# Performance work log

Measured on AMD Instinct MI355X. Metric: run time of the kernel, lower is better.

## Reference

```python
import jax, jax.numpy as jnp
import numpy as np

V, BLOCK, L, H, E, B, T = 1024, 2048, 4, 8, 512, 4, 2048
D = E // H  # head dim = 64

def setup_inputs() -> dict:
    key = jax.random.key(0)
    ks = jax.random.split(key, 8)
    s = 0.02
    return {
        "idx": jax.random.randint(ks[0], (B, T), 0, V),
        "wte": jax.random.normal(ks[1], (V, E), jnp.float32) * s,
        "wpe": jax.random.normal(ks[2], (BLOCK, E), jnp.float32) * s,
        "ln1_w": jnp.ones((L, E), jnp.float32),
        "ln1_b": jnp.zeros((L, E), jnp.float32),
        "attn_w": jax.random.normal(ks[3], (L, 3 * E, E), jnp.float32) * s,
        "attn_b": jnp.zeros((L, 3 * E), jnp.float32),
        "proj_w": jax.random.normal(ks[4], (L, E, E), jnp.float32) * s,
        "proj_b": jnp.zeros((L, E), jnp.float32),
        "ln2_w": jnp.ones((L, E), jnp.float32),
        "ln2_b": jnp.zeros((L, E), jnp.float32),
        "fc_w": jax.random.normal(ks[5], (L, 4 * E, E), jnp.float32) * s,
        "fc_b": jnp.zeros((L, 4 * E), jnp.float32),
        "fc2_w": jax.random.normal(ks[6], (L, E, 4 * E), jnp.float32) * s,
        "fc2_b": jnp.zeros((L, E), jnp.float32),
        "lnf_w": jnp.ones((E,), jnp.float32),
        "lnf_b": jnp.zeros((E,), jnp.float32),
    }

def layer_norm(x, w, b, eps=1e-5):
    mu = jnp.mean(x, axis=-1, keepdims=True)
    var = jnp.var(x, axis=-1, keepdims=True)
    return (x - mu) * jax.lax.rsqrt(var + eps) * w + b

def reference(idx, wte, wpe, ln1_w, ln1_b, attn_w, attn_b, proj_w, proj_b,
              ln2_w, ln2_b, fc_w, fc_b, fc2_w, fc2_b, lnf_w, lnf_b):
    b, t = idx.shape
    x = wte[idx] + wpe[:t]  # (B,T,E)
    causal = jnp.tril(jnp.ones((t, t), bool))
    scale = 1.0 / np.sqrt(D)

    def block(x, p):
        l1w, l1b, aw, ab, pw, pb, l2w, l2b, fw, fb, f2w, f2b = p
        h = layer_norm(x, l1w, l1b)
        qkv = h @ aw.T + ab  # (B,T,3E)
        q, k, v = jnp.split(qkv, 3, axis=-1)
        q = q.reshape(b, t, H, D)
        k = k.reshape(b, t, H, D)
        v = v.reshape(b, t, H, D)
        att = jnp.einsum('bqhd,bkhd->bhqk', q, k) * scale
        att = jnp.where(causal, att, -jnp.inf)
        att = jax.nn.softmax(att, axis=-1)
        y = jnp.einsum('bhqk,bkhd->bqhd', att, v).reshape(b, t, E)
        x = x + y @ pw.T + pb
        h2 = layer_norm(x, l2w, l2b)
        h2 = jax.nn.gelu(h2 @ fw.T + fb, approximate=False)
        x = x + h2 @ f2w.T + f2b
        return x, None

    params = (ln1_w, ln1_b, attn_w, attn_b, proj_w, proj_b,
              ln2_w, ln2_b, fc_w, fc_b, fc2_w, fc2_b)
    x, _ = jax.lax.scan(block, x, params)
    x = layer_norm(x, lnf_w, lnf_b)
    logits = x @ wte.T  # tied lm_head
    return logits
```

## Files before the change

kernel.cpp:

```cpp
#include <hip/hip_runtime.h>
#include <hip/hip_bf16.h>
#include <math.h>

#define B_ 4
#define T_ 2048
#define E_ 512
#define H_ 8
#define D_ 64
#define L_ 4
#define V_ 1024
#define NROWS (B_*T_)
#define KBLK 64
#define KVPAD 72
#define PPAD 72

typedef __hip_bfloat16 bf16;
typedef __attribute__((ext_vector_type(8))) short bf16x8;
typedef __attribute__((ext_vector_type(4))) float f32x4;

__device__ __forceinline__ short f2bf_s(float f) {
    union { bf16 h; short s; } t; t.h = __float2bfloat16(f); return t.s;
}

__device__ __forceinline__ void gload_lds16(const bf16* g, bf16* l) {
    __builtin_amdgcn_global_load_lds((const __attribute__((address_space(1))) void*)g,
                                     (__attribute__((address_space(3))) void*)l, 16, 0, 0);
}

__device__ __forceinline__ float gelu_fast(float v) {
    float u = v * (0.7978845608028654f * (1.0f + 0.044715f * v * v));
    float t = 1.0f - 2.0f / (__expf(2.0f * u) + 1.0f);
    return 0.5f * v * (1.0f + t);
}

__global__ void f2bf_all(const float* __restrict__ s0, const float* __restrict__ s1,
                         const float* __restrict__ s2, const float* __restrict__ s3,
                         const float* __restrict__ s4, bf16* __restrict__ dst) {
    size_t gi = (size_t)blockIdx.x * 1024 + threadIdx.x * 4;
    const float* src; size_t off;
    if (blockIdx.x < 3072)       { src = s0; off = gi; }
    else if (blockIdx.x < 4096)  { src = s1; off = gi - (size_t)3072 * 1024; }
    else if (blockIdx.x < 8192)  { src = s2; off = gi - (size_t)4096 * 1024; }
    else if (blockIdx.x < 12288) { src = s3; off = gi - (size_t)8192 * 1024; }
    else                         { src = s4; off = gi - (size_t)12288 * 1024; }
    float4 v = *(const float4*)(src + off);
    union { bf16 h[4]; uint2 u; } t;
    t.h[0] = __float2bfloat16(v.x); t.h[1] = __float2bfloat16(v.y);
    t.h[2] = __float2bfloat16(v.z); t.h[3] = __float2bfloat16(v.w);
    *(uint2*)(dst + gi) = t.u;
}

__global__ void embed_kernel(const int* __restrict__ idx, const float* __restrict__ wte,
                             const float* __restrict__ wpe, float* __restrict__ x) {
    int i = (blockIdx.x * blockDim.x + threadIdx.x) * 4;
    int row = i >> 9;
    int e = i & (E_ - 1);
    int t = row & (T_ - 1);
    int id = idx[row];
    float4 a = *(const float4*)(wte + (size_t)id * E_ + e);
    float4 p = *(const float4*)(wpe + (size_t)t * E_ + e);
    a.x += p.x; a.y += p.y; a.z += p.z; a.w += p.w;
    *(float4*)(x + i) = a;
}

__global__ __launch_bounds__(512) void layernorm_kernel(const float* __restrict__ x,
                                 const float* __restrict__ w, const float* __restrict__ b,
                                 bf16* __restrict__ out) {
    int wid = threadIdx.x >> 6, lane = threadIdx.x & 63;
    int row = blockIdx.x * 8 + wid;
    const float* xr = x + (size_t)row * E_ + lane * 8;
    float4 a0 = *(const float4*)xr;
    float4 a1 = *(const float4*)(xr + 4);
    float s = (a0.x + a0.y) + (a0.z + a0.w) + (a1.x + a1.y) + (a1.z + a1.w);
    float q = a0.x*a0.x + a0.y*a0.y + a0.z*a0.z + a0.w*a0.w
            + a1.x*a1.x + a1.y*a1.y + a1.z*a1.z + a1.w*a1.w;
    #pragma unroll
    for (int st = 1; st < 64; st <<= 1) { s += __shfl_xor(s, st); q += __shfl_xor(q, st); }
    float mean = s * (1.0f / E_);
    float var = q * (1.0f / E_) - mean * mean;
    float rstd = rsqrtf(var + 1e-5f);
    float4 w0 = *(const float4*)(w + lane * 8), w1 = *(const float4*)(w + lane * 8 + 4);
    float4 b0 = *(const float4*)(b + lane * 8), b1 = *(const float4*)(b + lane * 8 + 4);
    union { bf16 h[8]; uint4 u; } o;
    o.h[0] = __float2bfloat16((a0.x - mean) * rstd * w0.x + b0.x);
    o.h[1] = __float2bfloat16((a0.y - mean) * rstd * w0.y + b0.y);
    o.h[2] = __float2bfloat16((a0.z - mean) * rstd * w0.z + b0.z);
    o.h[3] = __float2bfloat16((a0.w - mean) * rstd * w0.w + b0.w);
    o.h[4] = __float2bfloat16((a1.x - mean) * rstd * w1.x + b1.x);
    o.h[5] = __float2bfloat16((a1.y - mean) * rstd * w1.y + b1.y);
    o.h[6] = __float2bfloat16((a1.z - mean) * rstd * w1.z + b1.z);
    o.h[7] = __float2bfloat16((a1.w - mean) * rstd * w1.w + b1.w);
    *(uint4*)(out + (size_t)row * E_ + lane * 8) = o.u;
}

template<int ACT, int OMODE, bool BIAS, bool QKV>
__global__ __launch_bounds__(256) void gemm_mfma(const bf16* __restrict__ A, const bf16* __restrict__ W,
        const float* __restrict__ bias, float* __restrict__ Cf, bf16* __restrict__ Cb,
        bf16* __restrict__ Vt, int M, int N, int K) {
    __shared__ __align__(16) bf16 As[2][128][32];
    __shared__ __align__(16) bf16 Bs[2][128][32];
    int tid = threadIdx.x;
    int lane = tid & 63, wid = tid >> 6;
    int wm = (wid >> 1) * 64, wn = (wid & 1) * 64;
    int m0 = blockIdx.y * 128, n0 = blockIdx.x * 128;

    int srow = wid * 32 + (lane >> 2);
    int scol = (lane & 3) * 8;
    const bf16* ga = A + (size_t)(m0 + srow) * K + scol;
    const bf16* gb = W + (size_t)(n0 + srow) * K + scol;
    int fr = lane & 15, fk = (lane >> 4) * 8;

    f32x4 acc[4][4];
    #pragma unroll
    for (int i = 0; i < 4; ++i)
        #pragma unroll
        for (int j = 0; j < 4; ++j) acc[i][j] = (f32x4){0.f, 0.f, 0.f, 0.f};

    gload_lds16(ga,          &As[0][wid * 32][0]);
    gload_lds16(ga + 16 * K, &As[0][wid * 32 + 16][0]);
    gload_lds16(gb,          &Bs[0][wid * 32][0]);
    gload_lds16(gb + 16 * K, &Bs[0][wid * 32 + 16][0]);
    __syncthreads();

    const int nst = K >> 5;
    for (int t = 0; t < nst; ++t) {
        const int cur = t & 1;
        if (t + 1 < nst) {
            const bf16* ga2 = ga + (t + 1) * 32;
            const bf16* gb2 = gb + (t + 1) * 32;
            gload_lds16(ga2,          &As[cur ^ 1][wid * 32][0]);
            gload_lds16(ga2 + 16 * K, &As[cur ^ 1][wid * 32 + 16][0]);
            gload_lds16(gb2,          &Bs[cur ^ 1][wid * 32][0]);
            gload_lds16(gb2 + 16 * K, &Bs[cur ^ 1][wid * 32 + 16][0]);
        }
        bf16x8 af[4], bff[4];
        #pragma unroll
        for (int i = 0; i < 4; ++i) af[i]  = *(const bf16x8*)&As[cur][wm + i * 16 + fr][fk];
        #pragma unroll
        for (int j = 0; j < 4; ++j) bff[j] = *(const bf16x8*)&Bs[cur][wn + j * 16 + fr][fk];
        #pragma unroll
        for (int i = 0; i < 4; ++i)
            #pragma unroll
            for (int j = 0; j < 4; ++j)
                acc[i][j] = __builtin_amdgcn_mfma_f32_16x16x32_bf16(af[i], bff[j], acc[i][j], 0, 0, 0);
        __syncthreads();
    }

    int orow = m0 + wm + (lane >> 4) * 4;
    int ocol = n0 + wn + (lane & 15);

    if (QKV && n0 >= 2 * E_) {
        #pragma unroll
        for (int i = 0; i < 4; ++i) {
            int rowb = orow + i * 16;
            int bb = rowb >> 11;
            int t0 = rowb & (T_ - 1);
            #pragma unroll
            for (int j = 0; j < 4; ++j) {
                int col = ocol + j * 16;
                int dg = col - 2 * E_;
                int hh = dg >> 6, dd = dg & 63;
                float bv = BIAS ? bias[col] : 0.0f;
                union { bf16 h[4]; short4 s4; } pk;
                #pragma unroll
                for (int r = 0; r < 4; ++r)
                    pk.h[r] = __float2bfloat16(acc[i][j][r] + bv);
                *(short4*)&Vt[(((size_t)bb * H_ + hh) * D_ + dd) * T_ + t0] = pk.s4;
            }
        }
        return;
    }

    #pragma unroll
    for (int i = 0; i < 4; ++i) {
        #pragma unroll
        for (int j = 0; j < 4; ++j) {
            #pragma unroll
            for (int r = 0; r < 4; ++r) {
                int row = orow + i * 16 + r;
                int col = ocol + j * 16;
                float v = acc[i][j][r];
                if (BIAS) v += bias[col];
                if (ACT == 1) v = gelu_fast(v);
                if (QKV) {
                    if (col < E_) v *= 0.125f;
                    Cb[(size_t)row * (2 * E_) + col] = __float2bfloat16(v);
                } else {
                    size_t off = (size_t)row * N + col;
                    if (OMODE == 0) Cf[off] = v;
                    else if (OMODE == 1) Cb[off] = __float2bfloat16(v);
                    else Cf[off] += v;
                }
            }
        }
    }
}

template<int OMODE, bool BIAS>
__global__ __launch_bounds__(256) void gemm_mfma64(const bf16* __restrict__ A, const bf16* __restrict__ W,
        const float* __restrict__ bias, float* __restrict__ Cf, bf16* __restrict__ Cb,
        int M, int N, int K) {
    __shared__ __align__(16) bf16 As[2][64][32];
    __shared__ __align__(16) bf16 Bs[2][64][32];
    int tid = threadIdx.x;
    int lane = tid & 63, wid = tid >> 6;
    int wm = (wid >> 1) * 32, wn = (wid & 1) * 32;
    int m0 = blockIdx.y * 64, n0 = blockIdx.x * 64;

    int srow = wid * 16 + (lane >> 2);
    int scol = (lane & 3) * 8;
    const bf16* ga = A + (size_t)(m0 + srow) * K + scol;
    const bf16* gb = W + (size_t)(n0 + srow) * K + scol;
    int fr = lane & 15, fk = (lane >> 4) * 8;

    f32x4 acc[2][2];
    #pragma unroll
    for (int i = 0; i < 2; ++i)
        #pragma unroll
        for (int j = 0; j < 2; ++j) acc[i][j] = (f32x4){0.f, 0.f, 0.f, 0.f};

    gload_lds16(ga, &As[0][wid * 16][0]);
    gload_lds16(gb, &Bs[0][wid * 16][0]);
    __syncthreads();

    const int nst = K >> 5;
    for (int t = 0; t < nst; ++t) {
        const int cur = t & 1;
        if (t + 1 < nst) {
            gload_lds16(ga + (t + 1) * 32, &As[cur ^ 1][wid * 16][0]);
            gload_lds16(gb + (t + 1) * 32, &Bs[cur ^ 1][wid * 16][0]);
        }
        bf16x8 af[2], bff[2];
        #pragma unroll
        for (int i = 0; i < 2; ++i) af[i]  = *(const bf16x8*)&As[cur][wm + i * 16 + fr][fk];
        #pragma unroll
        for (int j = 0; j < 2; ++j) bff[j] = *(const bf16x8*)&Bs[cur][wn + j * 16 + fr][fk];
        #pragma unroll
        for (int i = 0; i < 2; ++i)
            #pragma unroll
            for (int j = 0; j < 2; ++j)
                acc[i][j] = __builtin_amdgcn_mfma_f32_16x16x32_bf16(af[i], bff[j], acc[i][j], 0, 0, 0);
        __syncthreads();
    }

    int orow = m0 + wm + (lane >> 4) * 4;
    int ocol = n0 + wn + (lane & 15);
    #pragma unroll
    for (int i = 0; i < 2; ++i) {
        #pragma unroll
        for (int j = 0; j < 2; ++j) {
            #pragma unroll
            for (int r = 0; r < 4; ++r) {
                int row = orow + i * 16 + r;
                int col = ocol + j * 16;
                float v = acc[i][j][r];
                if (BIAS) v += bias[col];
                size_t off = (size_t)row * N + col;
                if (OMODE == 0) Cf[off] = v;
                else if (OMODE == 1) Cb[off] = __float2bfloat16(v);
                else Cf[off] += v;
            }
        }
    }
}

template<bool DOMASK>
__device__ __forceinline__ void attn_tile(
        const short (&Ks)[KBLK][KVPAD], const short (&VsT)[D_][KVPAD],
        short (*Psw)[PPAD], const bf16x8 (&qf)[2],
        float& m_run, float& l_run, f32x4 (&accO)[4],
        int fr, int fg, int k0, int qrow) {
    f32x4 st[4];
    __builtin_amdgcn_s_setprio(1);
    #pragma unroll
    for (int j = 0; j < 4; ++j) {
        f32x4 a = (f32x4){0.f, 0.f, 0.f, 0.f};
        #pragma unroll
        for (int kk = 0; kk < 2; ++kk) {
            bf16x8 kf = *(const bf16x8*)&Ks[j * 16 + fr][kk * 32 + fg * 8];
            a = __builtin_amdgcn_mfma_f32_16x16x32_bf16(kf, qf[kk], a, 0, 0, 0);
        }
        st[j] = a;
    }
    __builtin_amdgcn_s_setprio(0);
    float mx = -INFINITY;
    #pragma unroll
    for (int j = 0; j < 4; ++j)
        #pragma unroll
        for (int r = 0; r < 4; ++r) {
            if (DOMASK && (k0 + j * 16 + fg * 4 + r > qrow)) st[j][r] = -INFINITY;
            mx = fmaxf(mx, st[j][r]);
        }
    mx = fmaxf(mx, __shfl_xor(mx, 16));
    mx = fmaxf(mx, __shfl_xor(mx, 32));
    if (!__all(mx <= m_run + 8.0f)) {
        float mnew = fmaxf(m_run, mx);
        float corr = __expf(m_run - mnew);
        l_run *= corr;
        #pragma unroll
        for (int r = 0; r < 4; ++r) {
            float cr = __shfl(corr, fg * 4 + r);
            #pragma unroll
            for (int n = 0; n < 4; ++n) accO[n][r] *= cr;
        }
        m_run = mnew;
    }
    float rl = 0.0f;
    #pragma unroll
    for (int j = 0; j < 4; ++j) {
        float p0 = __expf(st[j][0] - m_run), p1 = __expf(st[j][1] - m_run);
        float p2 = __expf(st[j][2] - m_run), p3 = __expf(st[j][3] - m_run);
        rl += (p0 + p1) + (p2 + p3);
        short4 pk;
        pk.x = f2bf_s(p0); pk.y = f2bf_s(p1); pk.z = f2bf_s(p2); pk.w = f2bf_s(p3);
        *(short4*)&Psw[fr][j * 16 + fg * 4] = pk;
    }
    rl += __shfl_xor(rl, 16);
    rl += __shfl_xor(rl, 32);
    l_run += rl;
    __builtin_amdgcn_s_setprio(1);
    bf16x8 pa[2];
    #pragma unroll
    for (int kk = 0; kk < 2; ++kk)
        pa[kk] = *(const bf16x8*)&Psw[fr][kk * 32 + fg * 8];
    #pragma unroll
    for (int n = 0; n < 4; ++n)
        #pragma unroll
        for (int kk = 0; kk < 2; ++kk) {
            bf16x8 vb = *(const bf16x8*)&VsT[n * 16 + fr][kk * 32 + fg * 8];
            accO[n] = __builtin_amdgcn_mfma_f32_16x16x32_bf16(pa[kk], vb, accO[n], 0, 0, 0);
        }
    __builtin_amdgcn_s_setprio(0);
}

__global__ __launch_bounds__(256, 4) void attn_mfma(const bf16* __restrict__ qk,
                                                    const bf16* __restrict__ vt,
                                                    bf16* __restrict__ y) {
    __shared__ __align__(16) short Ks[KBLK][KVPAD];
    __shared__ __align__(16) short VsT[D_][KVPAD];
    __shared__ __align__(16) short Ps[4][16][PPAD];
    const int qi = (gridDim.x - 1) - blockIdx.x;
    const int h = blockIdx.y, b = blockIdx.z;
    const int q0 = qi * 64;
    const int tid = threadIdx.x;
    const int lane = tid & 63, wid = tid >> 6;
    const int fr = lane & 15, fg = lane >> 4;
    const int qmin = q0 + wid * 16;
    const int qrow = qmin + fr;

    const int sr0 = tid >> 3;
    const int sc = (tid & 7) * 8;
    const bf16* kst = qk + (size_t)(b * T_ + sr0) * (2 * E_) + E_ + h * D_ + sc;
    const bf16* vst = vt + ((size_t)(b * H_ + h) * D_ + sr0) * T_ + sc;

    const bf16* qbase = qk + (size_t)(b * T_ + qrow) * (2 * E_) + h * D_;
    bf16x8 qf[2];
    #pragma unroll
    for (int kk = 0; kk < 2; ++kk)
        qf[kk] = *(const bf16x8*)(qbase + kk * 32 + fg * 8);

    float m_run = -INFINITY, l_run = 0.0f;
    f32x4 accO[4];
    #pragma unroll
    for (int n = 0; n < 4; ++n) accO[n] = (f32x4){0.f, 0.f, 0.f, 0.f};

    const int ntiles = qi + 1;

    {
        uint4 k0r = *(const uint4*)kst;
        uint4 k1r = *(const uint4*)(kst + 32 * (2 * E_));
        uint4 v0r = *(const uint4*)vst;
        uint4 v1r = *(const uint4*)(vst + 32 * T_);
        *(uint4*)&Ks[sr0][sc] = k0r;  *(uint4*)&Ks[sr0 + 32][sc] = k1r;
        *(uint4*)&VsT[sr0][sc] = v0r; *(uint4*)&VsT[sr0 + 32][sc] = v1r;
    }
    __syncthreads();

    for (int kt = 0; kt < ntiles; ++kt) {
        const bool have_next = (kt + 1 < ntiles);
        uint4 nk0, nk1, nv0, nv1;
        if (have_next) {
            const bf16* kn = kst + (size_t)(kt + 1) * KBLK * (2 * E_);
            const bf16* vn = vst + (kt + 1) * KBLK;
            nk0 = *(const uint4*)kn; nk1 = *(const uint4*)(kn + 32 * (2 * E_));
            nv0 = *(const uint4*)vn; nv1 = *(const uint4*)(vn + 32 * T_);
        }

        if (kt + 1 == ntiles)
            attn_tile<true >(Ks, VsT, Ps[wid], qf, m_run, l_run, accO, fr, fg, kt * KBLK, qrow);
        else
            attn_tile<false>(Ks, VsT, Ps[wid], qf, m_run, l_run, accO, fr, fg, kt * KBLK, qrow);

        __syncthreads();
        if (have_next) {
            *(uint4*)&Ks[sr0][sc] = nk0;  *(uint4*)&Ks[sr0 + 32][sc] = nk1;
            *(uint4*)&VsT[sr0][sc] = nv0; *(uint4*)&VsT[sr0 + 32][sc] = nv1;
            __syncthreads();
        }
    }

    float linv = 1.0f / l_run;
    #pragma unroll
    for (int r = 0; r < 4; ++r) {
        float lr = __shfl(linv, fg * 4 + r);
        int gq = qmin + fg * 4 + r;
        #pragma unroll
        for (int n = 0; n < 4; ++n)
            y[(size_t)(b * T_ + gq) * E_ + h * D_ + n * 16 + fr] =
                __float2bfloat16(accO[n][r] * lr);
    }
}

extern "C" void kernel_launch(void* const* d_in, const int* in_sizes, int n_in,
                              void* d_out, int out_size, void* d_ws, size_t ws_size,
                              hipStream_t stream) {
    const int*   idx    = (const int*)d_in[0];
    const float* wte    = (const float*)d_in[1];
    const float* wpe    = (const float*)d_in[2];
    const float* ln1_w  = (const float*)d_in[3];
    const float* ln1_b  = (const float*)d_in[4];
    const float* attn_w = (const float*)d_in[5];
    const float* attn_b = (const float*)d_in[6];
    const float* proj_w = (const float*)d_in[7];
    const float* proj_b = (const float*)d_in[8];
    const float* ln2_w  = (const float*)d_in[9];
    const float* ln2_b  = (const float*)d_in[10];
    const float* fc_w   = (const float*)d_in[11];
    const float* fc_b   = (const float*)d_in[12];
    const float* fc2_w  = (const float*)d_in[13];
    const float* fc2_b  = (const float*)d_in[14];
    const float* lnf_w  = (const float*)d_in[15];
    const float* lnf_b  = (const float*)d_in[16];
    float* out = (float*)d_out;

    float* x   = (float*)d_ws;
    bf16* hbf  = (bf16*)(x + (size_t)NROWS * E_);
    bf16* big  = hbf + (size_t)NROWS * E_;
    bf16* qkb  = big;
    bf16* vtb  = big + (size_t)NROWS * 2 * E_;
    bf16* wb   = big + (size_t)NROWS * 4 * E_;
    bf16* attn_wb = wb;
    bf16* proj_wb = attn_wb + (size_t)L_ * 3 * E_ * E_;
    bf16* fc_wb   = proj_wb + (size_t)L_ * E_ * E_;
    bf16* fc2_wb  = fc_wb   + (size_t)L_ * 4 * E_ * E_;
    bf16* wte_b   = fc2_wb  + (size_t)L_ * E_ * 4 * E_;

    f2bf_all<<<12800, 256, 0, stream>>>(attn_w, proj_w, fc_w, fc2_w, wte, wb);
    embed_kernel<<<NROWS * E_ / 1024, 256, 0, stream>>>(idx, wte, wpe, x);

    for (int l = 0; l < L_; ++l) {
        layernorm_kernel<<<NROWS / 8, 512, 0, stream>>>(x, ln1_w + l * E_, ln1_b + l * E_, hbf);
        gemm_mfma<0, 1, true, true><<<dim3(3 * E_ / 128, NROWS / 128), 256, 0, stream>>>(
            hbf, attn_wb + (size_t)l * 3 * E_ * E_, attn_b + l * 3 * E_, nullptr, qkb, vtb,
            NROWS, 3 * E_, E_);
        attn_mfma<<<dim3(T_ / 64, H_, B_), 256, 0, stream>>>(qkb, vtb, hbf);
        gemm_mfma64<2, true><<<dim3(E_ / 64, NROWS / 64), 256, 0, stream>>>(
            hbf, proj_wb + (size_t)l * E_ * E_, proj_b + l * E_, x, nullptr,
            NROWS, E_, E_);
        layernorm_kernel<<<NROWS / 8, 512, 0, stream>>>(x, ln2_w + l * E_, ln2_b + l * E_, hbf);
        gemm_mfma<1, 1, true, false><<<dim3(4 * E_ / 128, NROWS / 128), 256, 0, stream>>>(
            hbf, fc_wb + (size_t)l * 4 * E_ * E_, fc_b + l * 4 * E_, nullptr, big, nullptr,
            NROWS, 4 * E_, E_);
        gemm_mfma64<2, true><<<dim3(E_ / 64, NROWS / 64), 256, 0, stream>>>(
            big, fc2_wb + (size_t)l * E_ * 4 * E_, fc2_b + l * E_, x, nullptr,
            NROWS, E_, 4 * E_);
    }
    layernorm_kernel<<<NROWS / 8, 512, 0, stream>>>(x, lnf_w, lnf_b, hbf);
    gemm_mfma64<0, false><<<dim3(V_ / 64, NROWS / 64), 256, 0, stream>>>(
        hbf, wte_b, nullptr, out, nullptr, NROWS, V_, E_);
}
```

Baseline: 869.0 us.

## Double attention key block to 128 and move QKV GEMM to 64x64 tiles

The attention kernel now processes 128 keys per tile instead of 64, with wider V and P shared-memory buffers, four-chunk cooperative loads, and half as many tile iterations per query block. Occupancy is lowered from 4 to 3 blocks per SM. The QKV projection moves from the 128x128 GEMM to the 64x64 GEMM, which takes over the V-transpose epilogue, giving more blocks at lower per-block reuse. The goal is fewer barriers and loop overheads in attention and better load balance for QKV, at the cost of more registers and LDS per attention block and extra masked work on the diagonal tile.

```diff
diff --git a/kernel.cpp b/kernel.cpp
--- a/kernel.cpp
+++ b/kernel.cpp
@@ -10,9 +10,10 @@
 #define L_ 4
 #define V_ 1024
 #define NROWS (B_*T_)
-#define KBLK 64
+#define KBLK 128
 #define KVPAD 72
-#define PPAD 72
+#define VPAD 136
+#define PPAD 136
 
 typedef __hip_bfloat16 bf16;
 typedef __attribute__((ext_vector_type(8))) short bf16x8;
@@ -93,10 +94,10 @@
     *(uint4*)(out + (size_t)row * E_ + lane * 8) = o.u;
 }
 
-template<int ACT, int OMODE, bool BIAS, bool QKV>
+template<int ACT, int OMODE, bool BIAS>
 __global__ __launch_bounds__(256) void gemm_mfma(const bf16* __restrict__ A, const bf16* __restrict__ W,
         const float* __restrict__ bias, float* __restrict__ Cf, bf16* __restrict__ Cb,
-        bf16* __restrict__ Vt, int M, int N, int K) {
+        int M, int N, int K) {
     __shared__ __align__(16) bf16 As[2][128][32];
     __shared__ __align__(16) bf16 Bs[2][128][32];
     int tid = threadIdx.x;
@@ -148,15 +149,84 @@
 
     int orow = m0 + wm + (lane >> 4) * 4;
     int ocol = n0 + wn + (lane & 15);
+    #pragma unroll
+    for (int i = 0; i < 4; ++i) {
+        #pragma unroll
+        for (int j = 0; j < 4; ++j) {
+            #pragma unroll
+            for (int r = 0; r < 4; ++r) {
+                int row = orow + i * 16 + r;
+                int col = ocol + j * 16;
+                float v = acc[i][j][r];
+                if (BIAS) v += bias[col];
+                if (ACT == 1) v = gelu_fast(v);
+                size_t off = (size_t)row * N + col;
+                if (OMODE == 0) Cf[off] = v;
+                else if (OMODE == 1) Cb[off] = __float2bfloat16(v);
+                else Cf[off] += v;
+            }
+        }
+    }
+}
+
+template<int OMODE, bool BIAS, bool QKV>
+__global__ __launch_bounds__(256) void gemm_mfma64(const bf16* __restrict__ A, const bf16* __restrict__ W,
+        const float* __restrict__ bias, float* __restrict__ Cf, bf16* __restrict__ Cb,
+        bf16* __restrict__ Vt, int M, int N, int K) {
+    __shared__ __align__(16) bf16 As[2][64][32];
+    __shared__ __align__(16) bf16 Bs[2][64][32];
+    int tid = threadIdx.x;
+    int lane = tid & 63, wid = tid >> 6;
+    int wm = (wid >> 1) * 32, wn = (wid & 1) * 32;
+    int m0 = blockIdx.y * 64, n0 = blockIdx.x * 64;
+
+    int srow = wid * 16 + (lane >> 2);
+    int scol = (lane & 3) * 8;
+    const bf16* ga = A + (size_t)(m0 + srow) * K + scol;
+    const bf16* gb = W + (size_t)(n0 + srow) * K + scol;
+    int fr = lane & 15, fk = (lane >> 4) * 8;
+
+    f32x4 acc[2][2];
+    #pragma unroll
+    for (int i = 0; i < 2; ++i)
+        #pragma unroll
+        for (int j = 0; j < 2; ++j) acc[i][j] = (f32x4){0.f, 0.f, 0.f, 0.f};
+
+    gload_lds16(ga, &As[0][wid * 16][0]);
+    gload_lds16(gb, &Bs[0][wid * 16][0]);
+    __syncthreads();
+
+    const int nst = K >> 5;
+    for (int t = 0; t < nst; ++t) {
+        const int cur = t & 1;
+        if (t + 1 < nst) {
+            gload_lds16(ga + (t + 1) * 32, &As[cur ^ 1][wid * 16][0]);
+            gload_lds16(gb + (t + 1) * 32, &Bs[cur ^ 1][wid * 16][0]);
+        }
+        bf16x8 af[2], bff[2];
+        #pragma unroll
+        for (int i = 0; i < 2; ++i) af[i]  = *(const bf16x8*)&As[cur][wm + i * 16 + fr][fk];
+        #pragma unroll
+        for (int j = 0; j < 2; ++j) bff[j] = *(const bf16x8*)&Bs[cur][wn + j * 16 + fr][fk];
+        #pragma unroll
+        for (int i = 0; i < 2; ++i)
+            #pragma unroll
+            for (int j = 0; j < 2; ++j)
+                acc[i][j] = __builtin_amdgcn_mfma_f32_16x16x32_bf16(af[i], bff[j], acc[i][j], 0, 0, 0);
+        __syncthreads();
+    }
+
+    int orow = m0 + wm + (lane >> 4) * 4;
+    int ocol = n0 + wn + (lane & 15);
 
     if (QKV && n0 >= 2 * E_) {
         #pragma unroll
-        for (int i = 0; i < 4; ++i) {
+        for (int i = 0; i < 2; ++i) {
             int rowb = orow + i * 16;
             int bb = rowb >> 11;
             int t0 = rowb & (T_ - 1);
             #pragma unroll
-            for (int j = 0; j < 4; ++j) {
+            for (int j = 0; j < 2; ++j) {
                 int col = ocol + j * 16;
                 int dg = col - 2 * E_;
                 int hh = dg >> 6, dd = dg & 63;
@@ -172,16 +242,15 @@
     }
 
     #pragma unroll
-    for (int i = 0; i < 4; ++i) {
-        #pragma unroll
-        for (int j = 0; j < 4; ++j) {
+    for (int i = 0; i < 2; ++i) {
+        #pragma unroll
+        for (int j = 0; j < 2; ++j) {
             #pragma unroll
             for (int r = 0; r < 4; ++r) {
                 int row = orow + i * 16 + r;
                 int col = ocol + j * 16;
                 float v = acc[i][j][r];
                 if (BIAS) v += bias[col];
-                if (ACT == 1) v = gelu_fast(v);
                 if (QKV) {
                     if (col < E_) v *= 0.125f;
                     Cb[(size_t)row * (2 * E_) + col] = __float2bfloat16(v);
@@ -196,84 +265,16 @@
     }
 }
 
-template<int OMODE, bool BIAS>
-__global__ __launch_bounds__(256) void gemm_mfma64(const bf16* __restrict__ A, const bf16* __restrict__ W,
-        const float* __restrict__ bias, float* __restrict__ Cf, bf16* __restrict__ Cb,
-        int M, int N, int K) {
-    __shared__ __align__(16) bf16 As[2][64][32];
-    __shared__ __align__(16) bf16 Bs[2][64][32];
-    int tid = threadIdx.x;
-    int lane = tid & 63, wid = tid >> 6;
-    int wm = (wid >> 1) * 32, wn = (wid & 1) * 32;
-    int m0 = blockIdx.y * 64, n0 = blockIdx.x * 64;
-
-    int srow = wid * 16 + (lane >> 2);
-    int scol = (lane & 3) * 8;
-    const bf16* ga = A + (size_t)(m0 + srow) * K + scol;
-    const bf16* gb = W + (size_t)(n0 + srow) * K + scol;
-    int fr = lane & 15, fk = (lane >> 4) * 8;
-
-    f32x4 acc[2][2];
-    #pragma unroll
-    for (int i = 0; i < 2; ++i)
-        #pragma unroll
-        for (int j = 0; j < 2; ++j) acc[i][j] = (f32x4){0.f, 0.f, 0.f, 0.f};
-
-    gload_lds16(ga, &As[0][wid * 16][0]);
-    gload_lds16(gb, &Bs[0][wid * 16][0]);
-    __syncthreads();
-
-    const int nst = K >> 5;
-    for (int t = 0; t < nst; ++t) {
-        const int cur = t & 1;
-        if (t + 1 < nst) {
-            gload_lds16(ga + (t + 1) * 32, &As[cur ^ 1][wid * 16][0]);
-            gload_lds16(gb + (t + 1) * 32, &Bs[cur ^ 1][wid * 16][0]);
-        }
-        bf16x8 af[2], bff[2];
-        #pragma unroll
-        for (int i = 0; i < 2; ++i) af[i]  = *(const bf16x8*)&As[cur][wm + i * 16 + fr][fk];
-        #pragma unroll
-        for (int j = 0; j < 2; ++j) bff[j] = *(const bf16x8*)&Bs[cur][wn + j * 16 + fr][fk];
-        #pragma unroll
-        for (int i = 0; i < 2; ++i)
-            #pragma unroll
-            for (int j = 0; j < 2; ++j)
-                acc[i][j] = __builtin_amdgcn_mfma_f32_16x16x32_bf16(af[i], bff[j], acc[i][j], 0, 0, 0);
-        __syncthreads();
-    }
-
-    int orow = m0 + wm + (lane >> 4) * 4;
-    int ocol = n0 + wn + (lane & 15);
-    #pragma unroll
-    for (int i = 0; i < 2; ++i) {
-        #pragma unroll
-        for (int j = 0; j < 2; ++j) {
-            #pragma unroll
-            for (int r = 0; r < 4; ++r) {
-                int row = orow + i * 16 + r;
-                int col = ocol + j * 16;
-                float v = acc[i][j][r];
-                if (BIAS) v += bias[col];
-                size_t off = (size_t)row * N + col;
-                if (OMODE == 0) Cf[off] = v;
-                else if (OMODE == 1) Cb[off] = __float2bfloat16(v);
-                else Cf[off] += v;
-            }
-        }
-    }
-}
-
 template<bool DOMASK>
 __device__ __forceinline__ void attn_tile(
-        const short (&Ks)[KBLK][KVPAD], const short (&VsT)[D_][KVPAD],
+        const short (&Ks)[KBLK][KVPAD], const short (&VsT)[D_][VPAD],
         short (*Psw)[PPAD], const bf16x8 (&qf)[2],
         float& m_run, float& l_run, f32x4 (&accO)[4],
         int fr, int fg, int k0, int qrow) {
-    f32x4 st[4];
+    f32x4 st[8];
     __builtin_amdgcn_s_setprio(1);
     #pragma unroll
-    for (int j = 0; j < 4; ++j) {
+    for (int j = 0; j < 8; ++j) {
         f32x4 a = (f32x4){0.f, 0.f, 0.f, 0.f};
         #pragma unroll
         for (int kk = 0; kk < 2; ++kk) {
@@ -285,7 +286,7 @@
     __builtin_amdgcn_s_setprio(0);
     float mx = -INFINITY;
     #pragma unroll
-    for (int j = 0; j < 4; ++j)
+    for (int j = 0; j < 8; ++j)
         #pragma unroll
         for (int r = 0; r < 4; ++r) {
             if (DOMASK && (k0 + j * 16 + fg * 4 + r > qrow)) st[j][r] = -INFINITY;
@@ -307,7 +308,7 @@
     }
     float rl = 0.0f;
     #pragma unroll
-    for (int j = 0; j < 4; ++j) {
+    for (int j = 0; j < 8; ++j) {
         float p0 = __expf(st[j][0] - m_run), p1 = __expf(st[j][1] - m_run);
         float p2 = __expf(st[j][2] - m_run), p3 = __expf(st[j][3] - m_run);
         rl += (p0 + p1) + (p2 + p3);
@@ -319,25 +320,25 @@
     rl += __shfl_xor(rl, 32);
     l_run += rl;
     __builtin_amdgcn_s_setprio(1);
-    bf16x8 pa[2];
-    #pragma unroll
-    for (int kk = 0; kk < 2; ++kk)
+    bf16x8 pa[4];
+    #pragma unroll
+    for (int kk = 0; kk < 4; ++kk)
         pa[kk] = *(const bf16x8*)&Psw[fr][kk * 32 + fg * 8];
     #pragma unroll
     for (int n = 0; n < 4; ++n)
         #pragma unroll
-        for (int kk = 0; kk < 2; ++kk) {
+        for (int kk = 0; kk < 4; ++kk) {
             bf16x8 vb = *(const bf16x8*)&VsT[n * 16 + fr][kk * 32 + fg * 8];
             accO[n] = __builtin_amdgcn_mfma_f32_16x16x32_bf16(pa[kk], vb, accO[n], 0, 0, 0);
         }
     __builtin_amdgcn_s_setprio(0);
 }
 
-__global__ __launch_bounds__(256, 4) void attn_mfma(const bf16* __restrict__ qk,
+__global__ __launch_bounds__(256, 3) void attn_mfma(const bf16* __restrict__ qk,
                                                     const bf16* __restrict__ vt,
                                                     bf16* __restrict__ y) {
     __shared__ __align__(16) short Ks[KBLK][KVPAD];
-    __shared__ __align__(16) short VsT[D_][KVPAD];
+    __shared__ __align__(16) short VsT[D_][VPAD];
     __shared__ __align__(16) short Ps[4][16][PPAD];
     const int qi = (gridDim.x - 1) - blockIdx.x;
     const int h = blockIdx.y, b = blockIdx.z;
@@ -348,10 +349,12 @@
     const int qmin = q0 + wid * 16;
     const int qrow = qmin + fr;
 
-    const int sr0 = tid >> 3;
-    const int sc = (tid & 7) * 8;
-    const bf16* kst = qk + (size_t)(b * T_ + sr0) * (2 * E_) + E_ + h * D_ + sc;
-    const bf16* vst = vt + ((size_t)(b * H_ + h) * D_ + sr0) * T_ + sc;
+    const int kr0 = tid >> 3;
+    const int kc = (tid & 7) * 8;
+    const int dv0 = tid >> 4;
+    const int vc = (tid & 15) * 8;
+    const bf16* kst = qk + (size_t)(b * T_ + kr0) * (2 * E_) + E_ + h * D_ + kc;
+    const bf16* vst = vt + ((size_t)(b * H_ + h) * D_ + dv0) * T_ + vc;
 
     const bf16* qbase = qk + (size_t)(b * T_ + qrow) * (2 * E_) + h * D_;
     bf16x8 qf[2];
@@ -364,26 +367,30 @@
     #pragma unroll
     for (int n = 0; n < 4; ++n) accO[n] = (f32x4){0.f, 0.f, 0.f, 0.f};
 
-    const int ntiles = qi + 1;
+    const int ntiles = (qi + 2) >> 1;
 
     {
-        uint4 k0r = *(const uint4*)kst;
-        uint4 k1r = *(const uint4*)(kst + 32 * (2 * E_));
-        uint4 v0r = *(const uint4*)vst;
-        uint4 v1r = *(const uint4*)(vst + 32 * T_);
-        *(uint4*)&Ks[sr0][sc] = k0r;  *(uint4*)&Ks[sr0 + 32][sc] = k1r;
-        *(uint4*)&VsT[sr0][sc] = v0r; *(uint4*)&VsT[sr0 + 32][sc] = v1r;
+        #pragma unroll
+        for (int c = 0; c < 4; ++c) {
+            uint4 kr = *(const uint4*)(kst + (size_t)(c * 32) * (2 * E_));
+            uint4 vr = *(const uint4*)(vst + (size_t)(c * 16) * T_);
+            *(uint4*)&Ks[kr0 + c * 32][kc] = kr;
+            *(uint4*)&VsT[dv0 + c * 16][vc] = vr;
+        }
     }
     __syncthreads();
 
     for (int kt = 0; kt < ntiles; ++kt) {
         const bool have_next = (kt + 1 < ntiles);
-        uint4 nk0, nk1, nv0, nv1;
+        uint4 nk[4], nv[4];
         if (have_next) {
             const bf16* kn = kst + (size_t)(kt + 1) * KBLK * (2 * E_);
             const bf16* vn = vst + (kt + 1) * KBLK;
-            nk0 = *(const uint4*)kn; nk1 = *(const uint4*)(kn + 32 * (2 * E_));
-            nv0 = *(const uint4*)vn; nv1 = *(const uint4*)(vn + 32 * T_);
+            #pragma unroll
+            for (int c = 0; c < 4; ++c) {
+                nk[c] = *(const uint4*)(kn + (size_t)(c * 32) * (2 * E_));
+                nv[c] = *(const uint4*)(vn + (size_t)(c * 16) * T_);
+            }
         }
 
         if (kt + 1 == ntiles)
@@ -393,8 +400,11 @@
 
         __syncthreads();
         if (have_next) {
-            *(uint4*)&Ks[sr0][sc] = nk0;  *(uint4*)&Ks[sr0 + 32][sc] = nk1;
-            *(uint4*)&VsT[sr0][sc] = nv0; *(uint4*)&VsT[sr0 + 32][sc] = nv1;
+            #pragma unroll
+            for (int c = 0; c < 4; ++c) {
+                *(uint4*)&Ks[kr0 + c * 32][kc] = nk[c];
+                *(uint4*)&VsT[dv0 + c * 16][vc] = nv[c];
+            }
             __syncthreads();
         }
     }
@@ -450,22 +460,22 @@
 
     for (int l = 0; l < L_; ++l) {
         layernorm_kernel<<<NROWS / 8, 512, 0, stream>>>(x, ln1_w + l * E_, ln1_b + l * E_, hbf);
-        gemm_mfma<0, 1, true, true><<<dim3(3 * E_ / 128, NROWS / 128), 256, 0, stream>>>(
+        gemm_mfma64<1, true, true><<<dim3(3 * E_ / 64, NROWS / 64), 256, 0, stream>>>(
             hbf, attn_wb + (size_t)l * 3 * E_ * E_, attn_b + l * 3 * E_, nullptr, qkb, vtb,
             NROWS, 3 * E_, E_);
         attn_mfma<<<dim3(T_ / 64, H_, B_), 256, 0, stream>>>(qkb, vtb, hbf);
-        gemm_mfma64<2, true><<<dim3(E_ / 64, NROWS / 64), 256, 0, stream>>>(
-            hbf, proj_wb + (size_t)l * E_ * E_, proj_b + l * E_, x, nullptr,
+        gemm_mfma64<2, true, false><<<dim3(E_ / 64, NROWS / 64), 256, 0, stream>>>(
+            hbf, proj_wb + (size_t)l * E_ * E_, proj_b + l * E_, x, nullptr, nullptr,
             NROWS, E_, E_);
         layernorm_kernel<<<NROWS / 8, 512, 0, stream>>>(x, ln2_w + l * E_, ln2_b + l * E_, hbf);
-        gemm_mfma<1, 1, true, false><<<dim3(4 * E_ / 128, NROWS / 128), 256, 0, stream>>>(
-            hbf, fc_wb + (size_t)l * 4 * E_ * E_, fc_b + l * 4 * E_, nullptr, big, nullptr,
+        gemm_mfma<1, 1, true><<<dim3(4 * E_ / 128, NROWS / 128), 256, 0, stream>>>(
+            hbf, fc_wb + (size_t)l * 4 * E_ * E_, fc_b + l * 4 * E_, nullptr, big,
             NROWS, 4 * E_, E_);
-        gemm_mfma64<2, true><<<dim3(E_ / 64, NROWS / 64), 256, 0, stream>>>(
-            big, fc2_wb + (size_t)l * E_ * 4 * E_, fc2_b + l * E_, x, nullptr,
+        gemm_mfma64<2, true, false><<<dim3(E_ / 64, NROWS / 64), 256, 0, stream>>>(
+            big, fc2_wb + (size_t)l * E_ * 4 * E_, fc2_b + l * E_, x, nullptr, nullptr,
             NROWS, E_, 4 * E_);
     }
     layernorm_kernel<<<NROWS / 8, 512, 0, stream>>>(x, lnf_w, lnf_b, hbf);
-    gemm_mfma64<0, false><<<dim3(V_ / 64, NROWS / 64), 256, 0, stream>>>(
-        hbf, wte_b, nullptr, out, nullptr, NROWS, V_, E_);
-}
+    gemm_mfma64<0, false, false><<<dim3(V_ / 64, NROWS / 64), 256, 0, stream>>>(
+        hbf, wte_b, nullptr, out, nullptr, nullptr, NROWS, V_, E_);
+}
```

After: 1.202 ms. 1.38x slower.

## Double-buffer attention K/V tiles and move QKV GEMM to 64x64 tiles

Applied to the files above, without the earlier changes.

The attention kernel now keeps two LDS buffers for K and V^T, so the next tile's registers are written into the spare buffer right after compute. This removes one of the two block barriers per iteration, at the cost of more shared memory and a lower occupancy hint (3 instead of 4 blocks). The QKV projection GEMM moves from the 128x128-tile kernel to the 64x64-tile kernel, with the QKV-specific epilogue (V transpose and Q scaling) carried over. That gives four times as many blocks and better CU fill, but less data reuse per block.

```diff
diff --git a/kernel.cpp b/kernel.cpp
--- a/kernel.cpp
+++ b/kernel.cpp
@@ -93,10 +93,10 @@
     *(uint4*)(out + (size_t)row * E_ + lane * 8) = o.u;
 }
 
-template<int ACT, int OMODE, bool BIAS, bool QKV>
+template<int ACT, int OMODE, bool BIAS>
 __global__ __launch_bounds__(256) void gemm_mfma(const bf16* __restrict__ A, const bf16* __restrict__ W,
         const float* __restrict__ bias, float* __restrict__ Cf, bf16* __restrict__ Cb,
-        bf16* __restrict__ Vt, int M, int N, int K) {
+        int M, int N, int K) {
     __shared__ __align__(16) bf16 As[2][128][32];
     __shared__ __align__(16) bf16 Bs[2][128][32];
     int tid = threadIdx.x;
@@ -148,15 +148,84 @@
 
     int orow = m0 + wm + (lane >> 4) * 4;
     int ocol = n0 + wn + (lane & 15);
+    #pragma unroll
+    for (int i = 0; i < 4; ++i) {
+        #pragma unroll
+        for (int j = 0; j < 4; ++j) {
+            #pragma unroll
+            for (int r = 0; r < 4; ++r) {
+                int row = orow + i * 16 + r;
+                int col = ocol + j * 16;
+                float v = acc[i][j][r];
+                if (BIAS) v += bias[col];
+                if (ACT == 1) v = gelu_fast(v);
+                size_t off = (size_t)row * N + col;
+                if (OMODE == 0) Cf[off] = v;
+                else if (OMODE == 1) Cb[off] = __float2bfloat16(v);
+                else Cf[off] += v;
+            }
+        }
+    }
+}
+
+template<int OMODE, bool BIAS, bool QKV>
+__global__ __launch_bounds__(256) void gemm_mfma64(const bf16* __restrict__ A, const bf16* __restrict__ W,
+        const float* __restrict__ bias, float* __restrict__ Cf, bf16* __restrict__ Cb,
+        bf16* __restrict__ Vt, int M, int N, int K) {
+    __shared__ __align__(16) bf16 As[2][64][32];
+    __shared__ __align__(16) bf16 Bs[2][64][32];
+    int tid = threadIdx.x;
+    int lane = tid & 63, wid = tid >> 6;
+    int wm = (wid >> 1) * 32, wn = (wid & 1) * 32;
+    int m0 = blockIdx.y * 64, n0 = blockIdx.x * 64;
+
+    int srow = wid * 16 + (lane >> 2);
+    int scol = (lane & 3) * 8;
+    const bf16* ga = A + (size_t)(m0 + srow) * K + scol;
+    const bf16* gb = W + (size_t)(n0 + srow) * K + scol;
+    int fr = lane & 15, fk = (lane >> 4) * 8;
+
+    f32x4 acc[2][2];
+    #pragma unroll
+    for (int i = 0; i < 2; ++i)
+        #pragma unroll
+        for (int j = 0; j < 2; ++j) acc[i][j] = (f32x4){0.f, 0.f, 0.f, 0.f};
+
+    gload_lds16(ga, &As[0][wid * 16][0]);
+    gload_lds16(gb, &Bs[0][wid * 16][0]);
+    __syncthreads();
+
+    const int nst = K >> 5;
+    for (int t = 0; t < nst; ++t) {
+        const int cur = t & 1;
+        if (t + 1 < nst) {
+            gload_lds16(ga + (t + 1) * 32, &As[cur ^ 1][wid * 16][0]);
+            gload_lds16(gb + (t + 1) * 32, &Bs[cur ^ 1][wid * 16][0]);
+        }
+        bf16x8 af[2], bff[2];
+        #pragma unroll
+        for (int i = 0; i < 2; ++i) af[i]  = *(const bf16x8*)&As[cur][wm + i * 16 + fr][fk];
+        #pragma unroll
+        for (int j = 0; j < 2; ++j) bff[j] = *(const bf16x8*)&Bs[cur][wn + j * 16 + fr][fk];
+        #pragma unroll
+        for (int i = 0; i < 2; ++i)
+            #pragma unroll
+            for (int j = 0; j < 2; ++j)
+                acc[i][j] = __builtin_amdgcn_mfma_f32_16x16x32_bf16(af[i], bff[j], acc[i][j], 0, 0, 0);
+        __syncthreads();
+    }
+
+    int orow = m0 + wm + (lane >> 4) * 4;
+    int ocol = n0 + wn + (lane & 15);
 
     if (QKV && n0 >= 2 * E_) {
         #pragma unroll
-        for (int i = 0; i < 4; ++i) {
+        for (int i = 0; i < 2; ++i) {
             int rowb = orow + i * 16;
             int bb = rowb >> 11;
             int t0 = rowb & (T_ - 1);
             #pragma unroll
-            for (int j = 0; j < 4; ++j) {
+            for (int j = 0; j < 2; ++j) {
                 int col = ocol + j * 16;
                 int dg = col - 2 * E_;
                 int hh = dg >> 6, dd = dg & 63;
@@ -172,16 +241,15 @@
     }
 
     #pragma unroll
-    for (int i = 0; i < 4; ++i) {
-        #pragma unroll
-        for (int j = 0; j < 4; ++j) {
+    for (int i = 0; i < 2; ++i) {
+        #pragma unroll
+        for (int j = 0; j < 2; ++j) {
             #pragma unroll
             for (int r = 0; r < 4; ++r) {
                 int row = orow + i * 16 + r;
                 int col = ocol + j * 16;
                 float v = acc[i][j][r];
                 if (BIAS) v += bias[col];
-                if (ACT == 1) v = gelu_fast(v);
                 if (QKV) {
                     if (col < E_) v *= 0.125f;
                     Cb[(size_t)row * (2 * E_) + col] = __float2bfloat16(v);
@@ -196,74 +264,6 @@
     }
 }
 
-template<int OMODE, bool BIAS>
-__global__ __launch_bounds__(256) void gemm_mfma64(const bf16* __restrict__ A, const bf16* __restrict__ W,
-        const float* __restrict__ bias, float* __restrict__ Cf, bf16* __restrict__ Cb,
-        int M, int N, int K) {
-    __shared__ __align__(16) bf16 As[2][64][32];
-    __shared__ __align__(16) bf16 Bs[2][64][32];
-    int tid = threadIdx.x;
-    int lane = tid & 63, wid = tid >> 6;
-    int wm = (wid >> 1) * 32, wn = (wid & 1) * 32;
-    int m0 = blockIdx.y * 64, n0 = blockIdx.x * 64;
-
-    int srow = wid * 16 + (lane >> 2);
-    int scol = (lane & 3) * 8;
-    const bf16* ga = A + (size_t)(m0 + srow) * K + scol;
-    const bf16* gb = W + (size_t)(n0 + srow) * K + scol;
-    int fr = lane & 15, fk = (lane >> 4) * 8;
-
-    f32x4 acc[2][2];
-    #pragma unroll
-    for (int i = 0; i < 2; ++i)
-        #pragma unroll
-        for (int j = 0; j < 2; ++j) acc[i][j] = (f32x4){0.f, 0.f, 0.f, 0.f};
-
-    gload_lds16(ga, &As[0][wid * 16][0]);
-    gload_lds16(gb, &Bs[0][wid * 16][0]);
-    __syncthreads();
-
-    const int nst = K >> 5;
-    for (int t = 0; t < nst; ++t) {
-        const int cur = t & 1;
-        if (t + 1 < nst) {
-            gload_lds16(ga + (t + 1) * 32, &As[cur ^ 1][wid * 16][0]);
-            gload_lds16(gb + (t + 1) * 32, &Bs[cur ^ 1][wid * 16][0]);
-        }
-        bf16x8 af[2], bff[2];
-        #pragma unroll
-        for (int i = 0; i < 2; ++i) af[i]  = *(const bf16x8*)&As[cur][wm + i * 16 + fr][fk];
-        #pragma unroll
-        for (int j = 0; j < 2; ++j) bff[j] = *(const bf16x8*)&Bs[cur][wn + j * 16 + fr][fk];
-        #pragma unroll
-        for (int i = 0; i < 2; ++i)
-            #pragma unroll
-            for (int j = 0; j < 2; ++j)
-                acc[i][j] = __builtin_amdgcn_mfma_f32_16x16x32_bf16(af[i], bff[j], acc[i][j], 0, 0, 0);
-        __syncthreads();
-    }
-
-    int orow = m0 + wm + (lane >> 4) * 4;
-    int ocol = n0 + wn + (lane & 15);
-    #pragma unroll
-    for (int i = 0; i < 2; ++i) {
-        #pragma unroll
-        for (int j = 0; j < 2; ++j) {
-            #pragma unroll
-            for (int r = 0; r < 4; ++r) {
-                int row = orow + i * 16 + r;
-                int col = ocol + j * 16;
-                float v = acc[i][j][r];
-                if (BIAS) v += bias[col];
-                size_t off = (size_t)row * N + col;
-                if (OMODE == 0) Cf[off] = v;
-                else if (OMODE == 1) Cb[off] = __float2bfloat16(v);
-                else Cf[off] += v;
-            }
-        }
-    }
-}
-
 template<bool DOMASK>
 __device__ __forceinline__ void attn_tile(
         const short (&Ks)[KBLK][KVPAD], const short (&VsT)[D_][KVPAD],
@@ -333,11 +333,11 @@
     __builtin_amdgcn_s_setprio(0);
 }
 
-__global__ __launch_bounds__(256, 4) void attn_mfma(const bf16* __restrict__ qk,
+__global__ __launch_bounds__(256, 3) void attn_mfma(const bf16* __restrict__ qk,
                                                     const bf16* __restrict__ vt,
                                                     bf16* __restrict__ y) {
-    __shared__ __align__(16) short Ks[KBLK][KVPAD];
-    __shared__ __align__(16) short VsT[D_][KVPAD];
+    __shared__ __align__(16) short Ks[2][KBLK][KVPAD];
+    __shared__ __align__(16) short VsT[2][D_][KVPAD];
     __shared__ __align__(16) short Ps[4][16][PPAD];
     const int qi = (gridDim.x - 1) - blockIdx.x;
     const int h = blockIdx.y, b = blockIdx.z;
@@ -371,12 +371,13 @@
         uint4 k1r = *(const uint4*)(kst + 32 * (2 * E_));
         uint4 v0r = *(const uint4*)vst;
         uint4 v1r = *(const uint4*)(vst + 32 * T_);
-        *(uint4*)&Ks[sr0][sc] = k0r;  *(uint4*)&Ks[sr0 + 32][sc] = k1r;
-        *(uint4*)&VsT[sr0][sc] = v0r; *(uint4*)&VsT[sr0 + 32][sc] = v1r;
+        *(uint4*)&Ks[0][sr0][sc] = k0r;  *(uint4*)&Ks[0][sr0 + 32][sc] = k1r;
+        *(uint4*)&VsT[0][sr0][sc] = v0r; *(uint4*)&VsT[0][sr0 + 32][sc] = v1r;
     }
     __syncthreads();
 
     for (int kt = 0; kt < ntiles; ++kt) {
+        const int cur = kt & 1;
         const bool have_next = (kt + 1 < ntiles);
         uint4 nk0, nk1, nv0, nv1;
         if (have_next) {
@@ -387,16 +388,16 @@
         }
 
         if (kt + 1 == ntiles)
-            attn_tile<true >(Ks, VsT, Ps[wid], qf, m_run, l_run, accO, fr, fg, kt * KBLK, qrow);
+            attn_tile<true >(Ks[cur], VsT[cur], Ps[wid], qf, m_run, l_run, accO, fr, fg, kt * KBLK, qrow);
         else
-            attn_tile<false>(Ks, VsT, Ps[wid], qf, m_run, l_run, accO, fr, fg, kt * KBLK, qrow);
-
+            attn_tile<false>(Ks[cur], VsT[cur], Ps[wid], qf, m_run, l_run, accO, fr, fg, kt * KBLK, qrow);
+
+        if (have_next) {
+            const int nxt = cur ^ 1;
+            *(uint4*)&Ks[nxt][sr0][sc] = nk0;  *(uint4*)&Ks[nxt][sr0 + 32][sc] = nk1;
+            *(uint4*)&VsT[nxt][sr0][sc] = nv0; *(uint4*)&VsT[nxt][sr0 + 32][sc] = nv1;
+        }
         __syncthreads();
-        if (have_next) {
-            *(uint4*)&Ks[sr0][sc] = nk0;  *(uint4*)&Ks[sr0 + 32][sc] = nk1;
-            *(uint4*)&VsT[sr0][sc] = nv0; *(uint4*)&VsT[sr0 + 32][sc] = nv1;
-            __syncthreads();
-        }
     }
 
     float linv = 1.0f / l_run;
@@ -450,22 +451,22 @@
 
     for (int l = 0; l < L_; ++l) {
         layernorm_kernel<<<NROWS / 8, 512, 0, stream>>>(x, ln1_w + l * E_, ln1_b + l * E_, hbf);
-        gemm_mfma<0, 1, true, true><<<dim3(3 * E_ / 128, NROWS / 128), 256, 0, stream>>>(
+        gemm_mfma64<1, true, true><<<dim3(3 * E_ / 64, NROWS / 64), 256, 0, stream>>>(
             hbf, attn_wb + (size_t)l * 3 * E_ * E_, attn_b + l * 3 * E_, nullptr, qkb, vtb,
             NROWS, 3 * E_, E_);
         attn_mfma<<<dim3(T_ / 64, H_, B_), 256, 0, stream>>>(qkb, vtb, hbf);
-        gemm_mfma64<2, true><<<dim3(E_ / 64, NROWS / 64), 256, 0, stream>>>(
-            hbf, proj_wb + (size_t)l * E_ * E_, proj_b + l * E_, x, nullptr,
+        gemm_mfma64<2, true, false><<<dim3(E_ / 64, NROWS / 64), 256, 0, stream>>>(
+            hbf, proj_wb + (size_t)l * E_ * E_, proj_b + l * E_, x, nullptr, nullptr,
             NROWS, E_, E_);
         layernorm_kernel<<<NROWS / 8, 512, 0, stream>>>(x, ln2_w + l * E_, ln2_b + l * E_, hbf);
-        gemm_mfma<1, 1, true, false><<<dim3(4 * E_ / 128, NROWS / 128), 256, 0, stream>>>(
-            hbf, fc_wb + (size_t)l * 4 * E_ * E_, fc_b + l * 4 * E_, nullptr, big, nullptr,
+        gemm_mfma<1, 1, true><<<dim3(4 * E_ / 128, NROWS / 128), 256, 0, stream>>>(
+            hbf, fc_wb + (size_t)l * 4 * E_ * E_, fc_b + l * 4 * E_, nullptr, big,
             NROWS, 4 * E_, E_);
-        gemm_mfma64<2, true><<<dim3(E_ / 64, NROWS / 64), 256, 0, stream>>>(
-            big, fc2_wb + (size_t)l * E_ * 4 * E_, fc2_b + l * E_, x, nullptr,
+        gemm_mfma64<2, true, false><<<dim3(E_ / 64, NROWS / 64), 256, 0, stream>>>(
+            big, fc2_wb + (size_t)l * E_ * 4 * E_, fc2_b + l * E_, x, nullptr, nullptr,
             NROWS, E_, 4 * E_);
     }
     layernorm_kernel<<<NROWS / 8, 512, 0, stream>>>(x, lnf_w, lnf_b, hbf);
-    gemm_mfma64<0, false><<<dim3(V_ / 64, NROWS / 64), 256, 0, stream>>>(
-        hbf, wte_b, nullptr, out, nullptr, NROWS, V_, E_);
-}
+    gemm_mfma64<0, false, false><<<dim3(V_ / 64, NROWS / 64), 256, 0, stream>>>(
+        hbf, wte_b, nullptr, out, nullptr, nullptr, NROWS, V_, E_);
+}
```

Measured after the change: 955.8 us. 1.1x slower.
